# Kernel optimization log

Measured on AMD Instinct MI355X. Metric: run time of the kernel, lower is better.

Reference implementation:

```python
import jax, jax.numpy as jnp
import numpy as np

CELL = 4  # 2 ** cell_2_pow, cell_2_pow = 2
EPS = 1e-5


def conv2d(x, w, b):
    # 3x3 conv, padding 1, NCHW / OIHW
    y = jax.lax.conv_general_dilated(
        x, w, window_strides=(1, 1), padding=((1, 1), (1, 1)),
        dimension_numbers=('NCHW', 'OIHW', 'NCHW'))
    return y + b[None, :, None, None]


def setup_inputs() -> dict:
    key = jax.random.key(0)
    ks = jax.random.split(key, 4)
    B, Cc, H, W = 8, 128, 512, 512
    nh, nw = H // CELL, W // CELL  # ctrl spatial must be padded_img / cell_sz
    return dict(
        image_pipe=jax.random.normal(ks[0], (B, 6, H, W), jnp.float32),
        ctrl_pipe=jax.random.normal(ks[1], (B, Cc, nh, nw), jnp.float32),
        w1=jax.random.normal(ks[2], (50, Cc, 3, 3), jnp.float32) * 0.03,
        b1=jnp.zeros((50,), jnp.float32),
        gamma=jnp.ones((50,), jnp.float32),
        beta=jnp.zeros((50,), jnp.float32),
        mean=jnp.zeros((50,), jnp.float32),
        var=jnp.ones((50,), jnp.float32),
        w2=jax.random.normal(ks[3], (18, 50, 3, 3), jnp.float32) * 0.05,
        b2=jnp.zeros((18,), jnp.float32),
    )


def reference(image_pipe, ctrl_pipe, w1, b1, gamma, beta, mean, var, w2, b2):
    cs = CELL
    B, C6, H, W = image_pipe.shape
    # conv_condense: Conv(Cc->50) -> ReLU -> BatchNorm2d(50, inference) -> Conv(50->18)
    h = jax.nn.relu(conv2d(ctrl_pipe, w1, b1))
    scale = gamma * jax.lax.rsqrt(var + EPS)
    h = (h - mean[None, :, None, None]) * scale[None, :, None, None] + beta[None, :, None, None]
    cond = conv2d(h, w2, b2)  # [B, 18, nh, nw]
    nh, nw = cond.shape[-2], cond.shape[-1]

    padH = (-H) % cs
    padW = (-W) % cs
    rH, rW = H + padH, W + padW
    # F.pad(img, (cell, padW+cell, cell, padH+cell)): left/right then top/bottom
    img = jnp.pad(image_pipe, ((0, 0), (0, 0), (cs, padH + cs), (cs, padW + cs)))

    # 9 cell-strided shifted views; torch loop order: i over width (outer), j over height (inner)
    stack = jnp.stack(
        [img[:, :, j * cs:j * cs + rH, i * cs:i * cs + rW]
         for i in range(3) for j in range(3)], axis=-1)  # [B, 6, rH, rW, 9]
    stack = stack.reshape(B, 2, 3, rH, rW, 9)  # 2 groups of 3 channels

    # per-pixel dynamic 9-tap weights, constant within each cs x cs cell
    wts = cond.reshape(B, 2, 9, nh, nw)
    wts = jnp.repeat(jnp.repeat(wts, cs, axis=3), cs, axis=4)  # [B, 2, 9, rH, rW]

    out = jnp.einsum('bgchwk,bgkhw->bgchw', stack, wts)  # weighted neighborhood sum
    out = out.reshape(B, 6, rH, rW)[:, :, :H, :W]
    return out
```

## Files before the change

### kernel.cpp

```cpp
#include <hip/hip_runtime.h>

typedef __attribute__((ext_vector_type(8))) short short8;
typedef __attribute__((ext_vector_type(4))) float floatx4;

__device__ __forceinline__ unsigned short f2bf(float f) {
    union { float f; unsigned int u; } v; v.f = f;
    unsigned int r = (v.u + 0x7fffu + ((v.u >> 16) & 1u)) >> 16;
    return (unsigned short)r;
}

__device__ __forceinline__ float4 shfl4(float4 v, int srcLane) {
    float4 r;
    r.x = __shfl(v.x, srcLane, 64);
    r.y = __shfl(v.y, srcLane, 64);
    r.z = __shfl(v.z, srcLane, 64);
    r.w = __shfl(v.w, srcLane, 64);
    return r;
}

__global__ __launch_bounds__(256) void transpose_kernel(
    const float* __restrict__ ctrl, unsigned short* __restrict__ ctrlT)
{
    __shared__ unsigned short tile[64 * 66];
    const int t = threadIdx.x;
    const int x0 = blockIdx.x * 64, ci0 = blockIdx.y * 64;
    const int b = blockIdx.z >> 7, y = blockIdx.z & 127;
#pragma unroll
    for (int it = 0; it < 4; it++) {
        int ci_l = it * 16 + (t >> 4);
        int x_l = (t & 15) * 4;
        const float4 v = *(const float4*)&ctrl[(((size_t)b * 128 + ci0 + ci_l) * 128 + y) * 128 + x0 + x_l];
        tile[(x_l + 0) * 66 + ci_l] = f2bf(v.x);
        tile[(x_l + 1) * 66 + ci_l] = f2bf(v.y);
        tile[(x_l + 2) * 66 + ci_l] = f2bf(v.z);
        tile[(x_l + 3) * 66 + ci_l] = f2bf(v.w);
    }
    __syncthreads();
#pragma unroll
    for (int it = 0; it < 2; it++) {
        int x_l = it * 32 + (t >> 3);
        int ci_l = (t & 7) * 8;
        const unsigned int* p = (const unsigned int*)&tile[x_l * 66 + ci_l];
        uint4 u = make_uint4(p[0], p[1], p[2], p[3]);
        *(uint4*)&ctrlT[(((size_t)b * 128 + y) * 128 + x0 + x_l) * 128 + ci0 + ci_l] = u;
    }
}

__global__ __launch_bounds__(256) void prep_w_kernel(
    const float* __restrict__ w1, const float* __restrict__ w2,
    unsigned short* __restrict__ w1p, unsigned short* __restrict__ w2p)
{
    int i = blockIdx.x * 256 + threadIdx.x;
    if (i < 4 * 9 * 64 * 32) {
        int ci = i & 31; int t2 = i >> 5; int co = t2 & 63; int t3 = t2 >> 6;
        int tap = t3 % 9; int c4 = t3 / 9;
        float v = 0.f;
        if (co < 50) v = w1[((size_t)co * 128 + c4 * 32 + ci) * 9 + tap];
        w1p[i] = f2bf(v);
    } else {
        int j = i - 4 * 9 * 64 * 32;
        int ci = j & 31; int t2 = j >> 5; int co = t2 & 31; int t3 = t2 >> 5;
        int tap = t3 % 9; int c4 = t3 / 9;
        int cig = c4 * 32 + ci;
        float v = 0.f;
        if (co < 18 && cig < 50) v = w2[((size_t)co * 50 + cig) * 9 + tap];
        w2p[j] = f2bf(v);
    }
}

__global__ __launch_bounds__(256) void conv1_mfma(
    const unsigned short* __restrict__ xT, const unsigned short* __restrict__ w1p,
    const float* __restrict__ b1, const float* __restrict__ gamma,
    const float* __restrict__ beta, const float* __restrict__ mean,
    const float* __restrict__ var, unsigned short* __restrict__ h)
{
    __shared__ unsigned short in_s[324 * 40];
    __shared__ unsigned short w_s[9 * 64 * 40];
    const int tid = threadIdx.x;
    const int x0 = blockIdx.x * 16, y0 = blockIdx.y * 16, b = blockIdx.z;
    const int wid = tid >> 6, lane = tid & 63;
    const int ln = lane & 15, q = lane >> 4;

    floatx4 acc[4][4];
#pragma unroll
    for (int mt = 0; mt < 4; mt++)
#pragma unroll
        for (int nt = 0; nt < 4; nt++) acc[mt][nt] = (floatx4)(0.f);

    for (int c4 = 0; c4 < 4; c4++) {
        for (int i = tid; i < 1296; i += 256) {
            int p = i >> 2, g = i & 3;
            int gy = y0 + p / 18 - 1, gx = x0 + p % 18 - 1;
            uint4 v = make_uint4(0, 0, 0, 0);
            if (gy >= 0 && gy < 128 && gx >= 0 && gx < 128)
                v = *(const uint4*)&xT[(((size_t)b * 128 + gy) * 128 + gx) * 128 + c4 * 32 + g * 8];
            *(uint4*)&in_s[p * 40 + g * 8] = v;
        }
#pragma unroll
        for (int it = 0; it < 9; it++) {
            int f = it * 256 + tid;
            int g = f & 3, co = (f >> 2) & 63, tap = f >> 8;
            uint4 v = *(const uint4*)&w1p[(((size_t)c4 * 9 + tap) * 64 + co) * 32 + g * 8];
            *(uint4*)&w_s[(tap * 64 + co) * 40 + g * 8] = v;
        }
        __syncthreads();

#pragma unroll
        for (int tap = 0; tap < 9; tap++) {
            const int dy = tap / 3, dx = tap % 3;
            short8 a[4];
#pragma unroll
            for (int mt = 0; mt < 4; mt++)
                a[mt] = *(const short8*)&in_s[((wid * 4 + mt + dy) * 18 + ln + dx) * 40 + q * 8];
#pragma unroll
            for (int nt = 0; nt < 4; nt++) {
                short8 bf = *(const short8*)&w_s[(tap * 64 + nt * 16 + ln) * 40 + q * 8];
#pragma unroll
                for (int mt = 0; mt < 4; mt++)
                    acc[mt][nt] = __builtin_amdgcn_mfma_f32_16x16x32_bf16(a[mt], bf, acc[mt][nt], 0, 0, 0);
            }
        }
        __syncthreads();
    }

#pragma unroll
    for (int nt = 0; nt < 4; nt++) {
        int co = nt * 16 + ln;
        bool real = co < 50;
        float sc = 0.f, mn = 0.f, bt = 0.f, bs = 0.f;
        if (real) {
            sc = gamma[co] * rsqrtf(var[co] + 1e-5f);
            mn = mean[co]; bt = beta[co]; bs = b1[co];
        }
#pragma unroll
        for (int mt = 0; mt < 4; mt++) {
            int gy = y0 + wid * 4 + mt;
#pragma unroll
            for (int r = 0; r < 4; r++) {
                int px = q * 4 + r;
                float v = 0.f;
                if (real) {
                    float tv = fmaxf(acc[mt][nt][r] + bs, 0.f);
                    v = (tv - mn) * sc + bt;
                }
                h[(((size_t)b * 128 + gy) * 128 + x0 + px) * 64 + co] = f2bf(v);
            }
        }
    }
}

__global__ __launch_bounds__(256) void conv2_mfma(
    const unsigned short* __restrict__ hT, const unsigned short* __restrict__ w2p,
    const float* __restrict__ b2, float* __restrict__ cond)
{
    __shared__ unsigned short in_s[324 * 40];
    __shared__ unsigned short w_s[9 * 32 * 40];
    const int tid = threadIdx.x;
    const int x0 = blockIdx.x * 16, y0 = blockIdx.y * 16, b = blockIdx.z;
    const int wid = tid >> 6, lane = tid & 63;
    const int ln = lane & 15, q = lane >> 4;

    floatx4 acc[4][2];
#pragma unroll
    for (int mt = 0; mt < 4; mt++)
#pragma unroll
        for (int nt = 0; nt < 2; nt++) acc[mt][nt] = (floatx4)(0.f);

    for (int c4 = 0; c4 < 2; c4++) {
        for (int i = tid; i < 1296; i += 256) {
            int p = i >> 2, g = i & 3;
            int gy = y0 + p / 18 - 1, gx = x0 + p % 18 - 1;
            uint4 v = make_uint4(0, 0, 0, 0);
            if (gy >= 0 && gy < 128 && gx >= 0 && gx < 128)
                v = *(const uint4*)&hT[(((size_t)b * 128 + gy) * 128 + gx) * 64 + c4 * 32 + g * 8];
            *(uint4*)&in_s[p * 40 + g * 8] = v;
        }
#pragma unroll
        for (int it = 0; it < 5; it++) {
            int f = it * 256 + tid;
            if (f < 1152) {
                int g = f & 3, co = (f >> 2) & 31, tap = f >> 7;
                uint4 v = *(const uint4*)&w2p[(((size_t)c4 * 9 + tap) * 32 + co) * 32 + g * 8];
                *(uint4*)&w_s[(tap * 32 + co) * 40 + g * 8] = v;
            }
        }
        __syncthreads();

#pragma unroll
        for (int tap = 0; tap < 9; tap++) {
            const int dy = tap / 3, dx = tap % 3;
            short8 a[4];
#pragma unroll
            for (int mt = 0; mt < 4; mt++)
                a[mt] = *(const short8*)&in_s[((wid * 4 + mt + dy) * 18 + ln + dx) * 40 + q * 8];
#pragma unroll
            for (int nt = 0; nt < 2; nt++) {
                short8 bf = *(const short8*)&w_s[(tap * 32 + nt * 16 + ln) * 40 + q * 8];
#pragma unroll
                for (int mt = 0; mt < 4; mt++)
                    acc[mt][nt] = __builtin_amdgcn_mfma_f32_16x16x32_bf16(a[mt], bf, acc[mt][nt], 0, 0, 0);
            }
        }
        __syncthreads();
    }

#pragma unroll
    for (int nt = 0; nt < 2; nt++) {
        int co = nt * 16 + ln;
        if (co < 18) {
            float bs = b2[co];
            int gch = co / 9, k = co % 9;
            int iw = k / 3, jy = k % 3;
            int pos = gch * 12 + jy * 4 + iw;
#pragma unroll
            for (int mt = 0; mt < 4; mt++) {
                int gy = y0 + wid * 4 + mt;
#pragma unroll
                for (int r = 0; r < 4; r++) {
                    int px = q * 4 + r;
                    cond[(((size_t)b * 128 + gy) * 128 + x0 + px) * 24 + pos] = acc[mt][nt][r] + bs;
                }
            }
        }
    }
}

__global__ __launch_bounds__(256) void apply_kernel(
    const float* __restrict__ img, const float* __restrict__ cond,
    float* __restrict__ out)
{
    const int tid = threadIdx.x;
    const int xl = tid & 63, s = tid >> 6;
    const int x4 = blockIdx.x * 64 + xl;
    const int base = blockIdx.y * 16;
    const int b = blockIdx.z >> 1, g = blockIdx.z & 1;
    const int cyb = base >> 2;
    const int laneL = (xl + 63) & 63;
    const int laneR = (xl + 1) & 63;
    const bool isL = (xl == 0), isR = (xl == 63);

    const float* imgc[3];
#pragma unroll
    for (int cc = 0; cc < 3; cc++)
        imgc[cc] = &img[(((size_t)b * 6 + g * 3 + cc) * 512) * 512];

    float4 acc[3][3];
#pragma unroll
    for (int sl = 0; sl < 3; sl++)
#pragma unroll
        for (int c = 0; c < 3; c++) acc[sl][c] = make_float4(0.f, 0.f, 0.f, 0.f);

    float4 vc[3], ec[3], vn[3], en[3];

    auto load_m = [&](int m, float4 vv[3], float4 ee[3]) {
        const int r = base + s + 4 * (m - 1);
        if (r >= 0 && r < 512) {
            const int xo = x4 * 4;
            const int xe = isL ? xo - 4 : xo + 4;
            const bool eok = (isL && x4 > 0) || (isR && x4 < 127);
#pragma unroll
            for (int cc = 0; cc < 3; cc++) {
                const float* rp = imgc[cc] + (size_t)r * 512;
                vv[cc] = *(const float4*)&rp[xo];
                ee[cc] = make_float4(0.f, 0.f, 0.f, 0.f);
                if (eok) ee[cc] = *(const float4*)&rp[xe];
            }
        } else {
#pragma unroll
            for (int cc = 0; cc < 3; cc++) {
                vv[cc] = make_float4(0.f, 0.f, 0.f, 0.f);
                ee[cc] = make_float4(0.f, 0.f, 0.f, 0.f);
            }
        }
    };

    load_m(0, vc, ec);

#pragma unroll
    for (int m = 0; m <= 5; m++) {
        if (m < 5) load_m(m + 1, vn, en);

        const int jlo = (m - 2 > 0) ? (m - 2) : 0;
        const int jhi = (m < 3) ? m : 3;

        float4 wv[3];
#pragma unroll
        for (int j = 0; j < 4; j++) {
            if (j >= jlo && j <= jhi) {
                const int jy = m - j;
                wv[j - jlo] = *(const float4*)&cond[
                    (((size_t)b * 128 + cyb + j) * 128 + x4) * 24 + g * 12 + jy * 4];
            }
        }

        float4 vL[3], vR[3];
#pragma unroll
        for (int cc = 0; cc < 3; cc++) {
            vL[cc] = shfl4(vc[cc], laneL);
            vR[cc] = shfl4(vc[cc], laneR);
            if (isL) vL[cc] = ec[cc];
            if (isR) vR[cc] = ec[cc];
        }

#pragma unroll
        for (int j = 0; j < 4; j++) {
            if (j >= jlo && j <= jhi) {
                const int slot = j % 3;
                const float4 w = wv[j - jlo];
#pragma unroll
                for (int cc = 0; cc < 3; cc++) {
                    acc[slot][cc].x += vL[cc].x * w.x + vc[cc].x * w.y + vR[cc].x * w.z;
                    acc[slot][cc].y += vL[cc].y * w.x + vc[cc].y * w.y + vR[cc].y * w.z;
                    acc[slot][cc].z += vL[cc].z * w.x + vc[cc].z * w.y + vR[cc].z * w.z;
                    acc[slot][cc].w += vL[cc].w * w.x + vc[cc].w * w.y + vR[cc].w * w.z;
                }
            }
        }

        const int jd = m - 2;
        if (jd >= 0) {
            const int o = base + 4 * jd + s;
            const int slot = jd % 3;
#pragma unroll
            for (int cc = 0; cc < 3; cc++) {
                *(float4*)&out[((((size_t)b * 6 + g * 3 + cc) * 512) + o) * 512 + x4 * 4] = acc[slot][cc];
                acc[slot][cc] = make_float4(0.f, 0.f, 0.f, 0.f);
            }
        }

        if (m < 5) {
#pragma unroll
            for (int cc = 0; cc < 3; cc++) { vc[cc] = vn[cc]; ec[cc] = en[cc]; }
        }
    }
}

extern "C" void kernel_launch(void* const* d_in, const int* in_sizes, int n_in,
                              void* d_out, int out_size, void* d_ws, size_t ws_size,
                              hipStream_t stream)
{
    const float* img   = (const float*)d_in[0];
    const float* ctrl  = (const float*)d_in[1];
    const float* w1    = (const float*)d_in[2];
    const float* b1    = (const float*)d_in[3];
    const float* gamma = (const float*)d_in[4];
    const float* beta  = (const float*)d_in[5];
    const float* mean  = (const float*)d_in[6];
    const float* var   = (const float*)d_in[7];
    const float* w2    = (const float*)d_in[8];
    const float* b2    = (const float*)d_in[9];
    float* out = (float*)d_out;

    char* ws = (char*)d_ws;
    unsigned short* ctrlT = (unsigned short*)ws;
    float*          cond  = (float*)ws;
    unsigned short* hbuf  = (unsigned short*)(ws + 33554432);
    unsigned short* w1p   = (unsigned short*)(ws + 50331648);
    unsigned short* w2p   = (unsigned short*)(ws + 50479104);

    transpose_kernel<<<dim3(2, 2, 1024), 256, 0, stream>>>(ctrl, ctrlT);
    prep_w_kernel<<<360, 256, 0, stream>>>(w1, w2, w1p, w2p);
    conv1_mfma<<<dim3(8, 8, 8), 256, 0, stream>>>(ctrlT, w1p, b1, gamma, beta, mean, var, hbuf);
    conv2_mfma<<<dim3(8, 8, 8), 256, 0, stream>>>(hbuf, w2p, b2, cond);
    apply_kernel<<<dim3(2, 32, 16), 256, 0, stream>>>(img, cond, out);
}
```

Baseline: 225.6 us.

## Double-buffer conv input tiles via registers and read weights directly from global

Both MFMA conv kernels now prefetch the next channel chunk's input halo into registers while computing the current chunk, then write it to a second LDS buffer. This overlaps global loads with MFMA work and removes one barrier per chunk. The weight tile is no longer staged in shared memory; B fragments are read straight from global memory, relying on cache hits. That frees LDS but adds global load latency inside the inner MFMA loop and raises register pressure from the staging array.

```diff
diff --git a/kernel.cpp b/kernel.cpp
--- a/kernel.cpp
+++ b/kernel.cpp
@@ -74,8 +74,7 @@
     const float* __restrict__ beta, const float* __restrict__ mean,
     const float* __restrict__ var, unsigned short* __restrict__ h)
 {
-    __shared__ unsigned short in_s[324 * 40];
-    __shared__ unsigned short w_s[9 * 64 * 40];
+    __shared__ unsigned short in_s[2][324 * 40];
     const int tid = threadIdx.x;
     const int x0 = blockIdx.x * 16, y0 = blockIdx.y * 16, b = blockIdx.z;
     const int wid = tid >> 6, lane = tid & 63;
@@ -87,39 +86,55 @@
 #pragma unroll
         for (int nt = 0; nt < 4; nt++) acc[mt][nt] = (floatx4)(0.f);
 
+    uint4 st[6];
+    auto stage_load = [&](int c4) {
+#pragma unroll
+        for (int k = 0; k < 6; k++) {
+            int i = tid + k * 256;
+            if (i < 1296) {
+                int p = i >> 2, g = i & 3;
+                int gy = y0 + p / 18 - 1, gx = x0 + p % 18 - 1;
+                st[k] = make_uint4(0, 0, 0, 0);
+                if (gy >= 0 && gy < 128 && gx >= 0 && gx < 128)
+                    st[k] = *(const uint4*)&xT[(((size_t)b * 128 + gy) * 128 + gx) * 128 + c4 * 32 + g * 8];
+            }
+        }
+    };
+    auto stage_write = [&](int buf) {
+#pragma unroll
+        for (int k = 0; k < 6; k++) {
+            int i = tid + k * 256;
+            if (i < 1296) {
+                int p = i >> 2, g = i & 3;
+                *(uint4*)&in_s[buf][p * 40 + g * 8] = st[k];
+            }
+        }
+    };
+
+    stage_load(0);
+    stage_write(0);
+    __syncthreads();
+
     for (int c4 = 0; c4 < 4; c4++) {
-        for (int i = tid; i < 1296; i += 256) {
-            int p = i >> 2, g = i & 3;
-            int gy = y0 + p / 18 - 1, gx = x0 + p % 18 - 1;
-            uint4 v = make_uint4(0, 0, 0, 0);
-            if (gy >= 0 && gy < 128 && gx >= 0 && gx < 128)
-                v = *(const uint4*)&xT[(((size_t)b * 128 + gy) * 128 + gx) * 128 + c4 * 32 + g * 8];
-            *(uint4*)&in_s[p * 40 + g * 8] = v;
-        }
-#pragma unroll
-        for (int it = 0; it < 9; it++) {
-            int f = it * 256 + tid;
-            int g = f & 3, co = (f >> 2) & 63, tap = f >> 8;
-            uint4 v = *(const uint4*)&w1p[(((size_t)c4 * 9 + tap) * 64 + co) * 32 + g * 8];
-            *(uint4*)&w_s[(tap * 64 + co) * 40 + g * 8] = v;
-        }
-        __syncthreads();
-
+        const int cur = c4 & 1;
+        if (c4 < 3) stage_load(c4 + 1);
+        const unsigned short* wbase = &w1p[(size_t)c4 * 9 * 64 * 32];
 #pragma unroll
         for (int tap = 0; tap < 9; tap++) {
             const int dy = tap / 3, dx = tap % 3;
             short8 a[4];
 #pragma unroll
             for (int mt = 0; mt < 4; mt++)
-                a[mt] = *(const short8*)&in_s[((wid * 4 + mt + dy) * 18 + ln + dx) * 40 + q * 8];
+                a[mt] = *(const short8*)&in_s[cur][((wid * 4 + mt + dy) * 18 + ln + dx) * 40 + q * 8];
 #pragma unroll
             for (int nt = 0; nt < 4; nt++) {
-                short8 bf = *(const short8*)&w_s[(tap * 64 + nt * 16 + ln) * 40 + q * 8];
+                short8 bf = *(const short8*)&wbase[((size_t)(tap * 64 + nt * 16 + ln)) * 32 + q * 8];
 #pragma unroll
                 for (int mt = 0; mt < 4; mt++)
                     acc[mt][nt] = __builtin_amdgcn_mfma_f32_16x16x32_bf16(a[mt], bf, acc[mt][nt], 0, 0, 0);
             }
         }
+        if (c4 < 3) stage_write(cur ^ 1);
         __syncthreads();
     }
 
@@ -153,8 +168,7 @@
     const unsigned short* __restrict__ hT, const unsigned short* __restrict__ w2p,
     const float* __restrict__ b2, float* __restrict__ cond)
 {
-    __shared__ unsigned short in_s[324 * 40];
-    __shared__ unsigned short w_s[9 * 32 * 40];
+    __shared__ unsigned short in_s[2][324 * 40];
     const int tid = threadIdx.x;
     const int x0 = blockIdx.x * 16, y0 = blockIdx.y * 16, b = blockIdx.z;
     const int wid = tid >> 6, lane = tid & 63;
@@ -166,41 +180,55 @@
 #pragma unroll
         for (int nt = 0; nt < 2; nt++) acc[mt][nt] = (floatx4)(0.f);
 
+    uint4 st[6];
+    auto stage_load = [&](int c4) {
+#pragma unroll
+        for (int k = 0; k < 6; k++) {
+            int i = tid + k * 256;
+            if (i < 1296) {
+                int p = i >> 2, g = i & 3;
+                int gy = y0 + p / 18 - 1, gx = x0 + p % 18 - 1;
+                st[k] = make_uint4(0, 0, 0, 0);
+                if (gy >= 0 && gy < 128 && gx >= 0 && gx < 128)
+                    st[k] = *(const uint4*)&hT[(((size_t)b * 128 + gy) * 128 + gx) * 64 + c4 * 32 + g * 8];
+            }
+        }
+    };
+    auto stage_write = [&](int buf) {
+#pragma unroll
+        for (int k = 0; k < 6; k++) {
+            int i = tid + k * 256;
+            if (i < 1296) {
+                int p = i >> 2, g = i & 3;
+                *(uint4*)&in_s[buf][p * 40 + g * 8] = st[k];
+            }
+        }
+    };
+
+    stage_load(0);
+    stage_write(0);
+    __syncthreads();
+
     for (int c4 = 0; c4 < 2; c4++) {
-        for (int i = tid; i < 1296; i += 256) {
-            int p = i >> 2, g = i & 3;
-            int gy = y0 + p / 18 - 1, gx = x0 + p % 18 - 1;
-            uint4 v = make_uint4(0, 0, 0, 0);
-            if (gy >= 0 && gy < 128 && gx >= 0 && gx < 128)
-                v = *(const uint4*)&hT[(((size_t)b * 128 + gy) * 128 + gx) * 64 + c4 * 32 + g * 8];
-            *(uint4*)&in_s[p * 40 + g * 8] = v;
-        }
-#pragma unroll
-        for (int it = 0; it < 5; it++) {
-            int f = it * 256 + tid;
-            if (f < 1152) {
-                int g = f & 3, co = (f >> 2) & 31, tap = f >> 7;
-                uint4 v = *(const uint4*)&w2p[(((size_t)c4 * 9 + tap) * 32 + co) * 32 + g * 8];
-                *(uint4*)&w_s[(tap * 32 + co) * 40 + g * 8] = v;
-            }
-        }
-        __syncthreads();
-
+        const int cur = c4 & 1;
+        if (c4 < 1) stage_load(c4 + 1);
+        const unsigned short* wbase = &w2p[(size_t)c4 * 9 * 32 * 32];
 #pragma unroll
         for (int tap = 0; tap < 9; tap++) {
             const int dy = tap / 3, dx = tap % 3;
             short8 a[4];
 #pragma unroll
             for (int mt = 0; mt < 4; mt++)
-                a[mt] = *(const short8*)&in_s[((wid * 4 + mt + dy) * 18 + ln + dx) * 40 + q * 8];
+                a[mt] = *(const short8*)&in_s[cur][((wid * 4 + mt + dy) * 18 + ln + dx) * 40 + q * 8];
 #pragma unroll
             for (int nt = 0; nt < 2; nt++) {
-                short8 bf = *(const short8*)&w_s[(tap * 32 + nt * 16 + ln) * 40 + q * 8];
+                short8 bf = *(const short8*)&wbase[((size_t)(tap * 32 + nt * 16 + ln)) * 32 + q * 8];
 #pragma unroll
                 for (int mt = 0; mt < 4; mt++)
                     acc[mt][nt] = __builtin_amdgcn_mfma_f32_16x16x32_bf16(a[mt], bf, acc[mt][nt], 0, 0, 0);
             }
         }
+        if (c4 < 1) stage_write(cur ^ 1);
         __syncthreads();
     }
 
```

New measurement: 272.0 us. +20.6%, slower.
